# Performance work log

Measured on AMD Instinct MI355X. Metric: run time of the kernel, lower is better.

The kernel has to match this reference:

```python
import jax, jax.numpy as jnp
import numpy as np

IN, SD, PD, K = 34, 4, 22, 8
WIDTH, NUM_CLASSES, NCONV = 126, 6, 2
N, NGRAPH = 16384, 8
BATCH_OFFSET = 1e3  # separates graphs in learned coordinate space
BLOCK = 1024


def knn_idx(s, k, block=BLOCK):
    # brute-force kNN in blocks of query rows; s: [N, SD]
    n = s.shape[0]
    rows = s.reshape(n // block, block, s.shape[-1])
    def f(r):  # r: [block, SD]
        d2 = jnp.sum((r[:, None, :] - s[None, :, :]) ** 2, -1)  # [block, N]
        _, idx = jax.lax.top_k(-d2, k)
        return idx
    return jax.lax.map(f, rows).reshape(n, k)


def gravnet_conv(x, batch, Ws, bs, Wh, bh, Wo1, Wo2, bo2):
    # s: learned coordinates, offset per-graph so kNN never crosses graphs
    s = x @ Ws + bs + (batch.astype(x.dtype) * BATCH_OFFSET)[:, None]  # [N, SD]
    h = x @ Wh + bh                                                    # [N, PD]
    idx = knn_idx(jax.lax.stop_gradient(s), K)                         # [N, K]
    d2 = jnp.sum((s[:, None, :] - s[idx]) ** 2, -1)                    # [N, K]
    w = jnp.exp(-10.0 * d2)                                            # [N, K]
    msg = h[idx] * w[..., None]                                        # [N, K, PD]
    agg = jnp.concatenate([msg.mean(1), msg.max(1)], -1)               # [N, 2*PD]
    return x @ Wo1 + agg @ Wo2 + bo2                                   # [N, IN]


def setup_inputs() -> dict:
    key = jax.random.key(0)
    ks = jax.random.split(key, 12)
    def g(k, shape, fan_in):
        return jax.random.normal(k, shape, jnp.float32) * (fan_in ** -0.5)
    return {
        "x": jax.random.normal(ks[0], (N, IN), jnp.float32),
        "batch": jnp.sort(jax.random.randint(ks[1], (N,), 0, NGRAPH)),
        "Ws": g(ks[2], (NCONV, IN, SD), IN),
        "bs": jnp.zeros((NCONV, SD), jnp.float32),
        "Wh": g(ks[3], (NCONV, IN, PD), IN),
        "bh": jnp.zeros((NCONV, PD), jnp.float32),
        "Wo1": g(ks[4], (NCONV, IN, IN), IN),
        "Wo2": g(ks[5], (NCONV, 2 * PD, IN), 2 * PD),
        "bo2": jnp.zeros((NCONV, IN), jnp.float32),
        "W1": g(ks[6], (IN, WIDTH), IN),
        "b1": jnp.zeros((WIDTH,), jnp.float32),
        "W2": g(ks[7], (WIDTH, WIDTH), WIDTH),
        "b2": jnp.zeros((WIDTH,), jnp.float32),
        "W3": g(ks[8], (WIDTH, NUM_CLASSES), WIDTH),
        "b3": jnp.zeros((NUM_CLASSES,), jnp.float32),
    }


def reference(x, batch, Ws, bs, Wh, bh, Wo1, Wo2, bo2, W1, b1, W2, b2, W3, b3):
    # Faithful to original: input_ is never updated, each conv sees raw x,
    # only the last conv's embedding feeds the MLP head.
    embedding = x
    for i in range(NCONV):
        embedding = gravnet_conv(x, batch, Ws[i], bs[i], Wh[i], bh[i], Wo1[i], Wo2[i], bo2[i])
    hdd = jax.nn.elu(embedding @ W1 + b1)
    hdd = jax.nn.elu(hdd @ W2 + b2)
    return hdd @ W3 + b3  # [N, NUM_CLASSES]
```

## Files before the change

### kernel.cpp

```cpp
#include <hip/hip_runtime.h>
#include <math.h>
#include <float.h>

#define NPT     16384
#define IN_F    34
#define SDIM    4
#define PDIM    22
#define KNN     8
#define WIDTH   126
#define WPAD    128
#define NCLS    6
#define ROWS    32

typedef unsigned long long u64;

#define OFF_RANGES 0
#define OFF_S      256
#define OFF_H      (OFF_S  + NPT*SDIM*4)
#define OFF_KIDX   (OFF_H  + NPT*PDIM*4)
#define OFF_KW     (OFF_KIDX + NPT*KNN*4)

#define INITK_BITS 0x7f7fffffffffffffULL

__device__ __forceinline__ void ce(double& a, double& b) {
    double mn = __builtin_fmin(a, b);
    double mx = __builtin_fmax(a, b);
    a = mn; b = mx;
}
__device__ __forceinline__ double dmin64(double a, double b) {
    return __builtin_fmin(a, b);
}
__device__ __forceinline__ double pack_key(float d2, unsigned j) {
    return __longlong_as_double((long long)(((u64)__float_as_uint(d2) << 32) | j));
}

__device__ __forceinline__ void key_insert(double key, double* u) {
#pragma unroll
    for (int t = 0; t < KNN; ++t) {
        double mn = __builtin_fmin(key, u[t]);
        double mx = __builtin_fmax(key, u[t]);
        u[t] = mn;
        key  = mx;
    }
}

__device__ __forceinline__ float dist2(const float4 a, const float4 b) {
    float d0 = a.x - b.x;
    float d1 = a.y - b.y;
    float d2 = a.z - b.z;
    float d3 = a.w - b.w;
    return __fadd_rn(__fadd_rn(__fadd_rn(__fmul_rn(d0, d0),
                                         __fmul_rn(d1, d1)),
                               __fmul_rn(d2, d2)),
                     __fmul_rn(d3, d3));
}

#define BITONIC8(m0,m1,m2,m3,m4,m5,m6,m7) \
    ce(m0,m4); ce(m1,m5); ce(m2,m6); ce(m3,m7); \
    ce(m0,m2); ce(m1,m3); ce(m4,m6); ce(m5,m7); \
    ce(m0,m1); ce(m2,m3); ce(m4,m5); ce(m6,m7);

#define SORT8(k0,k1,k2,k3,k4,k5,k6,k7) \
    ce(k0,k1); ce(k2,k3); ce(k4,k5); ce(k6,k7); \
    ce(k0,k2); ce(k1,k3); ce(k4,k6); ce(k5,k7); \
    ce(k1,k2); ce(k5,k6); \
    ce(k0,k4); ce(k1,k5); ce(k2,k6); ce(k3,k7); \
    ce(k2,k4); ce(k3,k5); \
    ce(k1,k2); ce(k3,k4); ce(k5,k6);

__global__ __launch_bounds__(256) void k_sh(const float* __restrict__ x,
                                            const int* __restrict__ batch,
                                            const float* __restrict__ Ws,
                                            const float* __restrict__ bs,
                                            const float* __restrict__ Wh,
                                            const float* __restrict__ bh,
                                            float* __restrict__ S,
                                            float* __restrict__ H,
                                            int* __restrict__ ranges) {
    int t = blockIdx.x * blockDim.x + threadIdx.x;
    int i = t >> 5;
    int o = t & 31;
    if (i >= NPT) return;
    if (o == 31) {
        int b = batch[i];
        if (i == 0 || batch[i - 1] != b) ranges[b * 2]     = i;
        if (i == NPT - 1 || batch[i + 1] != b) ranges[b * 2 + 1] = i + 1;
        return;
    }
    const float* xr = x + (size_t)i * IN_F;
    if (o < SDIM) {
        float acc = 0.f;
        for (int k = 0; k < IN_F; ++k) acc += xr[k] * Ws[k * SDIM + o];
        S[(size_t)i * SDIM + o] = (acc + bs[o]) + 1000.f * (float)batch[i];
    } else if (o < SDIM + PDIM) {
        int p = o - SDIM;
        float acc = 0.f;
        for (int k = 0; k < IN_F; ++k) acc += xr[k] * Wh[k * PDIM + p];
        H[(size_t)i * PDIM + p] = acc + bh[p];
    }
}

__global__ __launch_bounds__(256, 4) void k_knn(const float4* __restrict__ S4,
                                                const int* __restrict__ batch,
                                                const int* __restrict__ ranges,
                                                int* __restrict__ KIDX,
                                                float* __restrict__ KW) {
    const int tid = threadIdx.x;
    const int q   = blockIdx.x * 8 + (tid >> 5);
    const int t   = tid & 31;
    const int b   = batch[q];
    const int gs  = ranges[b * 2];
    const int len = ranges[b * 2 + 1] - gs;
    const float4 sq = S4[q];

    double u[KNN];
    const double initk = __longlong_as_double((long long)INITK_BITS);
#pragma unroll
    for (int e = 0; e < KNN; ++e) u[e] = initk;

    int j = gs + t;
    int done = 0;

    const int nfull8 = len >> 8;
    for (int bb = 0; bb < nfull8; ++bb, j += 256) {
        const float4* p = S4 + j;
        float4 s0 = p[0];
        float4 s1 = p[32];
        float4 s2 = p[64];
        float4 s3 = p[96];
        float4 s4 = p[128];
        float4 s5 = p[160];
        float4 s6 = p[192];
        float4 s7 = p[224];
        double k0 = pack_key(dist2(sq, s0), (unsigned)(j));
        double k1 = pack_key(dist2(sq, s1), (unsigned)(j + 32));
        double k2 = pack_key(dist2(sq, s2), (unsigned)(j + 64));
        double k3 = pack_key(dist2(sq, s3), (unsigned)(j + 96));
        double k4 = pack_key(dist2(sq, s4), (unsigned)(j + 128));
        double k5 = pack_key(dist2(sq, s5), (unsigned)(j + 160));
        double k6 = pack_key(dist2(sq, s6), (unsigned)(j + 192));
        double k7 = pack_key(dist2(sq, s7), (unsigned)(j + 224));
        SORT8(k0, k1, k2, k3, k4, k5, k6, k7);
        double m0 = dmin64(k0, u[7]);
        double m1 = dmin64(k1, u[6]);
        double m2 = dmin64(k2, u[5]);
        double m3 = dmin64(k3, u[4]);
        double m4 = dmin64(k4, u[3]);
        double m5 = dmin64(k5, u[2]);
        double m6 = dmin64(k6, u[1]);
        double m7 = dmin64(k7, u[0]);
        BITONIC8(m0, m1, m2, m3, m4, m5, m6, m7);
        u[0] = m0; u[1] = m1; u[2] = m2; u[3] = m3;
        u[4] = m4; u[5] = m5; u[6] = m6; u[7] = m7;
    }
    done = nfull8 << 8;

    if (len - done >= 128) {
        const float4* p = S4 + j;
        float4 s0 = p[0];
        float4 s1 = p[32];
        float4 s2 = p[64];
        float4 s3 = p[96];
        double k0 = pack_key(dist2(sq, s0), (unsigned)(j));
        double k1 = pack_key(dist2(sq, s1), (unsigned)(j + 32));
        double k2 = pack_key(dist2(sq, s2), (unsigned)(j + 64));
        double k3 = pack_key(dist2(sq, s3), (unsigned)(j + 96));
        ce(k0, k1); ce(k2, k3); ce(k0, k2); ce(k1, k3); ce(k1, k2);
        double m0 = dmin64(k0, u[7]);
        double m1 = dmin64(k1, u[6]);
        double m2 = dmin64(k2, u[5]);
        double m3 = dmin64(k3, u[4]);
        double m4 = u[3], m5 = u[2], m6 = u[1], m7 = u[0];
        BITONIC8(m0, m1, m2, m3, m4, m5, m6, m7);
        u[0] = m0; u[1] = m1; u[2] = m2; u[3] = m3;
        u[4] = m4; u[5] = m5; u[6] = m6; u[7] = m7;
        done += 128;
    }

    for (int m = done + t; m < len; m += 32) {
        int jj = gs + m;
        key_insert(pack_key(dist2(sq, S4[jj]), (unsigned)jj), u);
    }

#pragma unroll
    for (int mm = 1; mm < 32; mm <<= 1) {
        double p0 = __shfl_xor(u[0], mm, 32);
        double p1 = __shfl_xor(u[1], mm, 32);
        double p2 = __shfl_xor(u[2], mm, 32);
        double p3 = __shfl_xor(u[3], mm, 32);
        double p4 = __shfl_xor(u[4], mm, 32);
        double p5 = __shfl_xor(u[5], mm, 32);
        double p6 = __shfl_xor(u[6], mm, 32);
        double p7 = __shfl_xor(u[7], mm, 32);
        double m0 = dmin64(u[0], p7);
        double m1 = dmin64(u[1], p6);
        double m2 = dmin64(u[2], p5);
        double m3 = dmin64(u[3], p4);
        double m4 = dmin64(u[4], p3);
        double m5 = dmin64(u[5], p2);
        double m6 = dmin64(u[6], p1);
        double m7 = dmin64(u[7], p0);
        BITONIC8(m0, m1, m2, m3, m4, m5, m6, m7);
        u[0] = m0; u[1] = m1; u[2] = m2; u[3] = m3;
        u[4] = m4; u[5] = m5; u[6] = m6; u[7] = m7;
    }

    if (t == 0) {
#pragma unroll
        for (int e = 0; e < KNN; ++e) {
            u64 bits = (u64)__double_as_longlong(u[e]);
            float d = __uint_as_float((unsigned)(bits >> 32));
            KIDX[(size_t)q * KNN + e] = (int)(unsigned)(bits & 0xffffffffu);
            KW[(size_t)q * KNN + e]   = expf(-10.f * d);
        }
    }
}

__global__ __launch_bounds__(512, 4) void k_fused(
        const float* __restrict__ x,
        const float* __restrict__ H,
        const int* __restrict__ KIDX,
        const float* __restrict__ KW,
        const float* __restrict__ Wo1,
        const float* __restrict__ Wo2,
        const float* __restrict__ bo2,
        const float* __restrict__ W1,
        const float* __restrict__ b1,
        const float* __restrict__ W2,
        const float* __restrict__ b2,
        const float* __restrict__ W3,
        const float* __restrict__ b3,
        float* __restrict__ out) {
    __shared__ float xt[ROWS * IN_F];
    __shared__ float aggt[ROWS * 2 * PDIM];
    __shared__ float et[ROWS * IN_F];
    __shared__ float h1t[ROWS * WPAD];
    __shared__ float wbuf[2 * 32 * WPAD];
    __shared__ float w3buf[WPAD * NCLS];

    const int tid  = threadIdx.x;
    const int r    = tid >> 4;
    const int c    = tid & 15;
    const int row0 = blockIdx.x * ROWS;
    const int gi   = row0 + r;
    const int jA   = 4 * c;
    const int jB   = 64 + 4 * c;

    for (int t = tid; t < ROWS * IN_F; t += 512)
        xt[t] = x[(size_t)row0 * IN_F + t];
    for (int t = tid; t < IN_F * WPAD; t += 512) {
        int k = t >> 7, j = t & 127;
        wbuf[(k >> 5) * (32 * WPAD) + (k & 31) * WPAD + j] =
            (j < WIDTH) ? W1[k * WIDTH + j] : 0.f;
    }
    for (int t = tid; t < WPAD * NCLS; t += 512) {
        int k = t / NCLS;
        w3buf[t] = (k < WIDTH) ? W3[t] : 0.f;
    }

    if (c < 11) {
        const int p0 = c, p1 = c + 11;
        float s0 = 0.f, s1 = 0.f;
        float m0 = -FLT_MAX, m1 = -FLT_MAX;
#pragma unroll
        for (int k = 0; k < KNN; ++k) {
            int   j = KIDX[(size_t)gi * KNN + k];
            float w = KW[(size_t)gi * KNN + k];
            const float* hr = H + (size_t)j * PDIM;
            float v0 = hr[p0] * w; s0 += v0; m0 = fmaxf(m0, v0);
            float v1 = hr[p1] * w; s1 += v1; m1 = fmaxf(m1, v1);
        }
        aggt[r * 44 + p0] = s0 * 0.125f; aggt[r * 44 + PDIM + p0] = m0;
        aggt[r * 44 + p1] = s1 * 0.125f; aggt[r * 44 + PDIM + p1] = m1;
    }
    __syncthreads();

    float rvA[8], rvB[8];
#pragma unroll
    for (int i = 0; i < 8; ++i) {
        int e = i * 512 + tid, kk = e >> 7, j = e & 127;
        rvA[i] = (j < WIDTH) ? W2[(size_t)kk * WIDTH + j] : 0.f;
    }

    {
        const int j0 = (3 * c < 31) ? 3 * c : 31;
        float acc[3] = {0.f, 0.f, 0.f};
        const float* ar = xt + r * IN_F;
#pragma unroll 4
        for (int k = 0; k < IN_F; ++k) {
            float av = ar[k];
            const float* wr = Wo1 + k * IN_F + j0;
#pragma unroll
            for (int jj = 0; jj < 3; ++jj) acc[jj] += av * wr[jj];
        }
        const float* gr = aggt + r * 44;
#pragma unroll 4
        for (int p = 0; p < 2 * PDIM; ++p) {
            float av = gr[p];
            const float* wr = Wo2 + p * IN_F + j0;
#pragma unroll
            for (int jj = 0; jj < 3; ++jj) acc[jj] += av * wr[jj];
        }
#pragma unroll
        for (int jj = 0; jj < 3; ++jj)
            et[r * IN_F + j0 + jj] = acc[jj] + bo2[j0 + jj];
    }
    __syncthreads();

    {
        float aA[4] = {0.f, 0.f, 0.f, 0.f};
        float aB[4] = {0.f, 0.f, 0.f, 0.f};
        const float* ar = et + r * IN_F;
#pragma unroll 4
        for (int k = 0; k < IN_F; ++k) {
            float av = ar[k];
            const float* wr = wbuf + (k >> 5) * (32 * WPAD) + (k & 31) * WPAD;
            const float4 wA = *(const float4*)(wr + jA);
            const float4 wB = *(const float4*)(wr + jB);
            aA[0] += av * wA.x; aA[1] += av * wA.y;
            aA[2] += av * wA.z; aA[3] += av * wA.w;
            aB[0] += av * wB.x; aB[1] += av * wB.y;
            aB[2] += av * wB.z; aB[3] += av * wB.w;
        }
#pragma unroll
        for (int jj = 0; jj < 4; ++jj) {
            float vA = aA[jj] + b1[jA + jj];
            h1t[r * WPAD + jA + jj] = vA > 0.f ? vA : expm1f(vA);
            int j = jB + jj;
            float vB = aB[jj] + b1[j < WIDTH ? j : WIDTH - 1];
            h1t[r * WPAD + j] = (j < WIDTH) ? (vB > 0.f ? vB : expm1f(vB)) : 0.f;
        }
    }
    __syncthreads();

    float aA[4] = {0.f, 0.f, 0.f, 0.f};
    float aB[4] = {0.f, 0.f, 0.f, 0.f};
    const float* ar = h1t + r * WPAD;

#define STORE_CHUNK(BUFI, RV)                                   \
    _Pragma("unroll")                                           \
    for (int i = 0; i < 8; ++i)                                 \
        wbuf[(BUFI) * 4096 + i * 512 + tid] = RV[i];

#define LOAD_CHUNK(RV, K0)                                      \
    _Pragma("unroll")                                           \
    for (int i = 0; i < 8; ++i) {                               \
        int e = i * 512 + tid, kk = e >> 7, j = e & 127;        \
        int row = (K0) + kk;                                    \
        RV[i] = (j < WIDTH && row < WIDTH)                      \
                    ? W2[(size_t)row * WIDTH + j] : 0.f;        \
    }

#define COMPUTE_CHUNK(BUFI, K0)                                 \
    {                                                           \
        const float* wb = wbuf + (BUFI) * 4096;                 \
        _Pragma("unroll 4")                                     \
        for (int k = 0; k < 32; ++k) {                          \
            float av = ar[(K0) + k];                            \
            const float4 wA = *(const float4*)(wb + k * WPAD + jA); \
            const float4 wB = *(const float4*)(wb + k * WPAD + jB); \
            aA[0] += av * wA.x; aA[1] += av * wA.y;             \
            aA[2] += av * wA.z; aA[3] += av * wA.w;             \
            aB[0] += av * wB.x; aB[1] += av * wB.y;             \
            aB[2] += av * wB.z; aB[3] += av * wB.w;             \
        }                                                       \
    }

    STORE_CHUNK(0, rvA);  LOAD_CHUNK(rvB, 32);
    __syncthreads();
    COMPUTE_CHUNK(0, 0);
    STORE_CHUNK(1, rvB);  LOAD_CHUNK(rvA, 64);
    __syncthreads();
    COMPUTE_CHUNK(1, 32);
    STORE_CHUNK(0, rvA);  LOAD_CHUNK(rvB, 96);
    __syncthreads();
    COMPUTE_CHUNK(0, 64);
    STORE_CHUNK(1, rvB);
    __syncthreads();
    COMPUTE_CHUNK(1, 96);

    {
        float pc[NCLS] = {0.f, 0.f, 0.f, 0.f, 0.f, 0.f};
#pragma unroll
        for (int jj = 0; jj < 4; ++jj) {
            int ja = jA + jj;
            float vA = aA[jj] + b2[ja];
            float hA = vA > 0.f ? vA : expm1f(vA);
            const float* w3a = w3buf + ja * NCLS;
#pragma unroll
            for (int cc = 0; cc < NCLS; ++cc) pc[cc] += hA * w3a[cc];
            int jb = jB + jj;
            float vB = aB[jj] + b2[jb < WIDTH ? jb : WIDTH - 1];
            float hB = (jb < WIDTH) ? (vB > 0.f ? vB : expm1f(vB)) : 0.f;
            const float* w3b = w3buf + jb * NCLS;
#pragma unroll
            for (int cc = 0; cc < NCLS; ++cc) pc[cc] += hB * w3b[cc];
        }
#pragma unroll
        for (int mm = 1; mm < 16; mm <<= 1) {
#pragma unroll
            for (int cc = 0; cc < NCLS; ++cc)
                pc[cc] += __shfl_xor(pc[cc], mm, 16);
        }
        if (c == 0) {
#pragma unroll
            for (int cc = 0; cc < NCLS; ++cc)
                out[(size_t)gi * NCLS + cc] = pc[cc] + b3[cc];
        }
    }
#undef STORE_CHUNK
#undef LOAD_CHUNK
#undef COMPUTE_CHUNK
}

extern "C" void kernel_launch(void* const* d_in, const int* in_sizes, int n_in,
                              void* d_out, int out_size, void* d_ws, size_t ws_size,
                              hipStream_t stream) {
    const float* x     = (const float*)d_in[0];
    const int*   batch = (const int*)d_in[1];
    const float* Ws  = (const float*)d_in[2] + IN_F * SDIM;
    const float* bs  = (const float*)d_in[3] + SDIM;
    const float* Wh  = (const float*)d_in[4] + IN_F * PDIM;
    const float* bh  = (const float*)d_in[5] + PDIM;
    const float* Wo1 = (const float*)d_in[6] + IN_F * IN_F;
    const float* Wo2 = (const float*)d_in[7] + 2 * PDIM * IN_F;
    const float* bo2 = (const float*)d_in[8] + IN_F;
    const float* W1  = (const float*)d_in[9];
    const float* b1  = (const float*)d_in[10];
    const float* W2  = (const float*)d_in[11];
    const float* b2  = (const float*)d_in[12];
    const float* W3  = (const float*)d_in[13];
    const float* b3  = (const float*)d_in[14];
    float* out = (float*)d_out;

    char* ws = (char*)d_ws;
    int*   ranges = (int*)(ws + OFF_RANGES);
    float* S      = (float*)(ws + OFF_S);
    float* H      = (float*)(ws + OFF_H);
    int*   KIDX   = (int*)(ws + OFF_KIDX);
    float* KW     = (float*)(ws + OFF_KW);

    k_sh<<<dim3(NPT * 32 / 256), dim3(256), 0, stream>>>(x, batch, Ws, bs, Wh, bh, S, H, ranges);
    k_knn<<<dim3(NPT / 8), dim3(256), 0, stream>>>((const float4*)S, batch, ranges, KIDX, KW);
    k_fused<<<dim3(NPT / ROWS), dim3(512), 0, stream>>>(x, H, KIDX, KW, Wo1, Wo2, bo2,
                                                        W1, b1, W2, b2, W3, b3, out);
}
```

Baseline: 76.44 us.

## Pre-pad MLP weights in workspace and read them from global in fused head

W1 and W2 are now padded to 128 columns once per call by extra blocks appended to the first kernel, writing into workspace. The fused head kernel then reads the padded weights straight from global memory (L1/L2) instead of staging them through a double-buffered shared-memory pipeline with barriers. Rows per block are halved along with threads per block, which cuts shared memory use and may raise occupancy. The trade-off is that every block now rereads the weights from global or cache memory rather than shared memory.

```diff
diff --git a/kernel.cpp b/kernel.cpp
--- a/kernel.cpp
+++ b/kernel.cpp
@@ -10,15 +10,17 @@
 #define WIDTH   126
 #define WPAD    128
 #define NCLS    6
-#define ROWS    32
+#define ROWS    16
 
 typedef unsigned long long u64;
 
 #define OFF_RANGES 0
 #define OFF_S      256
-#define OFF_H      (OFF_S  + NPT*SDIM*4)
-#define OFF_KIDX   (OFF_H  + NPT*PDIM*4)
+#define OFF_H      (OFF_S    + NPT*SDIM*4)
+#define OFF_KIDX   (OFF_H    + NPT*PDIM*4)
 #define OFF_KW     (OFF_KIDX + NPT*KNN*4)
+#define OFF_W1P    (OFF_KW   + NPT*KNN*4)
+#define OFF_W2P    (OFF_W1P  + IN_F*WPAD*4)
 
 #define INITK_BITS 0x7f7fffffffffffffULL
 
@@ -68,15 +70,35 @@
     ce(k2,k4); ce(k3,k5); \
     ce(k1,k2); ce(k3,k4); ce(k5,k6);
 
+#define SH_BLOCKS  (NPT * 32 / 256)
+#define PAD_ELEMS  (IN_F * WPAD + WPAD * WPAD)
+#define PAD_BLOCKS ((PAD_ELEMS + 255) / 256)
+
 __global__ __launch_bounds__(256) void k_sh(const float* __restrict__ x,
                                             const int* __restrict__ batch,
                                             const float* __restrict__ Ws,
                                             const float* __restrict__ bs,
                                             const float* __restrict__ Wh,
                                             const float* __restrict__ bh,
+                                            const float* __restrict__ W1,
+                                            const float* __restrict__ W2,
                                             float* __restrict__ S,
                                             float* __restrict__ H,
+                                            float* __restrict__ W1P,
+                                            float* __restrict__ W2P,
                                             int* __restrict__ ranges) {
+    if (blockIdx.x >= SH_BLOCKS) {
+        int e = (blockIdx.x - SH_BLOCKS) * 256 + threadIdx.x;
+        if (e < IN_F * WPAD) {
+            int k = e >> 7, j = e & 127;
+            W1P[e] = (j < WIDTH) ? W1[k * WIDTH + j] : 0.f;
+        } else if (e < PAD_ELEMS) {
+            int e2 = e - IN_F * WPAD;
+            int k = e2 >> 7, j = e2 & 127;
+            W2P[e2] = (k < WIDTH && j < WIDTH) ? W2[(size_t)k * WIDTH + j] : 0.f;
+        }
+        return;
+    }
     int t = blockIdx.x * blockDim.x + threadIdx.x;
     int i = t >> 5;
     int o = t & 31;
@@ -216,7 +238,7 @@
     }
 }
 
-__global__ __launch_bounds__(512, 4) void k_fused(
+__global__ __launch_bounds__(256, 4) void k_fused(
         const float* __restrict__ x,
         const float* __restrict__ H,
         const int* __restrict__ KIDX,
@@ -224,9 +246,9 @@
         const float* __restrict__ Wo1,
         const float* __restrict__ Wo2,
         const float* __restrict__ bo2,
-        const float* __restrict__ W1,
+        const float* __restrict__ W1P,
         const float* __restrict__ b1,
-        const float* __restrict__ W2,
+        const float* __restrict__ W2P,
         const float* __restrict__ b2,
         const float* __restrict__ W3,
         const float* __restrict__ b3,
@@ -235,7 +257,6 @@
     __shared__ float aggt[ROWS * 2 * PDIM];
     __shared__ float et[ROWS * IN_F];
     __shared__ float h1t[ROWS * WPAD];
-    __shared__ float wbuf[2 * 32 * WPAD];
     __shared__ float w3buf[WPAD * NCLS];
 
     const int tid  = threadIdx.x;
@@ -246,14 +267,9 @@
     const int jA   = 4 * c;
     const int jB   = 64 + 4 * c;
 
-    for (int t = tid; t < ROWS * IN_F; t += 512)
+    for (int t = tid; t < ROWS * IN_F; t += 256)
         xt[t] = x[(size_t)row0 * IN_F + t];
-    for (int t = tid; t < IN_F * WPAD; t += 512) {
-        int k = t >> 7, j = t & 127;
-        wbuf[(k >> 5) * (32 * WPAD) + (k & 31) * WPAD + j] =
-            (j < WIDTH) ? W1[k * WIDTH + j] : 0.f;
-    }
-    for (int t = tid; t < WPAD * NCLS; t += 512) {
+    for (int t = tid; t < WPAD * NCLS; t += 256) {
         int k = t / NCLS;
         w3buf[t] = (k < WIDTH) ? W3[t] : 0.f;
     }
@@ -274,13 +290,6 @@
         aggt[r * 44 + p1] = s1 * 0.125f; aggt[r * 44 + PDIM + p1] = m1;
     }
     __syncthreads();
-
-    float rvA[8], rvB[8];
-#pragma unroll
-    for (int i = 0; i < 8; ++i) {
-        int e = i * 512 + tid, kk = e >> 7, j = e & 127;
-        rvA[i] = (j < WIDTH) ? W2[(size_t)kk * WIDTH + j] : 0.f;
-    }
 
     {
         const int j0 = (3 * c < 31) ? 3 * c : 31;
@@ -314,9 +323,8 @@
 #pragma unroll 4
         for (int k = 0; k < IN_F; ++k) {
             float av = ar[k];
-            const float* wr = wbuf + (k >> 5) * (32 * WPAD) + (k & 31) * WPAD;
-            const float4 wA = *(const float4*)(wr + jA);
-            const float4 wB = *(const float4*)(wr + jB);
+            const float4 wA = *(const float4*)(W1P + k * WPAD + jA);
+            const float4 wB = *(const float4*)(W1P + k * WPAD + jB);
             aA[0] += av * wA.x; aA[1] += av * wA.y;
             aA[2] += av * wA.z; aA[3] += av * wA.w;
             aB[0] += av * wB.x; aB[1] += av * wB.y;
@@ -333,53 +341,21 @@
     }
     __syncthreads();
 
-    float aA[4] = {0.f, 0.f, 0.f, 0.f};
-    float aB[4] = {0.f, 0.f, 0.f, 0.f};
-    const float* ar = h1t + r * WPAD;
-
-#define STORE_CHUNK(BUFI, RV)                                   \
-    _Pragma("unroll")                                           \
-    for (int i = 0; i < 8; ++i)                                 \
-        wbuf[(BUFI) * 4096 + i * 512 + tid] = RV[i];
-
-#define LOAD_CHUNK(RV, K0)                                      \
-    _Pragma("unroll")                                           \
-    for (int i = 0; i < 8; ++i) {                               \
-        int e = i * 512 + tid, kk = e >> 7, j = e & 127;        \
-        int row = (K0) + kk;                                    \
-        RV[i] = (j < WIDTH && row < WIDTH)                      \
-                    ? W2[(size_t)row * WIDTH + j] : 0.f;        \
-    }
-
-#define COMPUTE_CHUNK(BUFI, K0)                                 \
-    {                                                           \
-        const float* wb = wbuf + (BUFI) * 4096;                 \
-        _Pragma("unroll 4")                                     \
-        for (int k = 0; k < 32; ++k) {                          \
-            float av = ar[(K0) + k];                            \
-            const float4 wA = *(const float4*)(wb + k * WPAD + jA); \
-            const float4 wB = *(const float4*)(wb + k * WPAD + jB); \
-            aA[0] += av * wA.x; aA[1] += av * wA.y;             \
-            aA[2] += av * wA.z; aA[3] += av * wA.w;             \
-            aB[0] += av * wB.x; aB[1] += av * wB.y;             \
-            aB[2] += av * wB.z; aB[3] += av * wB.w;             \
-        }                                                       \
-    }
-
-    STORE_CHUNK(0, rvA);  LOAD_CHUNK(rvB, 32);
-    __syncthreads();
-    COMPUTE_CHUNK(0, 0);
-    STORE_CHUNK(1, rvB);  LOAD_CHUNK(rvA, 64);
-    __syncthreads();
-    COMPUTE_CHUNK(1, 32);
-    STORE_CHUNK(0, rvA);  LOAD_CHUNK(rvB, 96);
-    __syncthreads();
-    COMPUTE_CHUNK(0, 64);
-    STORE_CHUNK(1, rvB);
-    __syncthreads();
-    COMPUTE_CHUNK(1, 96);
-
     {
+        float aA[4] = {0.f, 0.f, 0.f, 0.f};
+        float aB[4] = {0.f, 0.f, 0.f, 0.f};
+        const float* ar = h1t + r * WPAD;
+#pragma unroll 4
+        for (int k = 0; k < WPAD; ++k) {
+            float av = ar[k];
+            const float4 wA = *(const float4*)(W2P + k * WPAD + jA);
+            const float4 wB = *(const float4*)(W2P + k * WPAD + jB);
+            aA[0] += av * wA.x; aA[1] += av * wA.y;
+            aA[2] += av * wA.z; aA[3] += av * wA.w;
+            aB[0] += av * wB.x; aB[1] += av * wB.y;
+            aB[2] += av * wB.z; aB[3] += av * wB.w;
+        }
+
         float pc[NCLS] = {0.f, 0.f, 0.f, 0.f, 0.f, 0.f};
 #pragma unroll
         for (int jj = 0; jj < 4; ++jj) {
@@ -408,9 +384,6 @@
                 out[(size_t)gi * NCLS + cc] = pc[cc] + b3[cc];
         }
     }
-#undef STORE_CHUNK
-#undef LOAD_CHUNK
-#undef COMPUTE_CHUNK
 }
 
 extern "C" void kernel_launch(void* const* d_in, const int* in_sizes, int n_in,
@@ -439,9 +412,12 @@
     float* H      = (float*)(ws + OFF_H);
     int*   KIDX   = (int*)(ws + OFF_KIDX);
     float* KW     = (float*)(ws + OFF_KW);
-
-    k_sh<<<dim3(NPT * 32 / 256), dim3(256), 0, stream>>>(x, batch, Ws, bs, Wh, bh, S, H, ranges);
+    float* W1P    = (float*)(ws + OFF_W1P);
+    float* W2P    = (float*)(ws + OFF_W2P);
+
+    k_sh<<<dim3(SH_BLOCKS + PAD_BLOCKS), dim3(256), 0, stream>>>(
+        x, batch, Ws, bs, Wh, bh, W1, W2, S, H, W1P, W2P, ranges);
     k_knn<<<dim3(NPT / 8), dim3(256), 0, stream>>>((const float4*)S, batch, ranges, KIDX, KW);
-    k_fused<<<dim3(NPT / ROWS), dim3(512), 0, stream>>>(x, H, KIDX, KW, Wo1, Wo2, bo2,
-                                                        W1, b1, W2, b2, W3, b3, out);
-}
+    k_fused<<<dim3(NPT / ROWS), dim3(256), 0, stream>>>(x, H, KIDX, KW, Wo1, Wo2, bo2,
+                                                        W1P, b1, W2P, b2, W3, b3, out);
+}
```

New measurement: 98.80 us. +29.3%, slower.
